# Kernel optimization log

Hardware: AMD Instinct MI355X
Metric: run time of the kernel (lower is better)

The kernel has to match this reference:

```python
import jax, jax.numpy as jnp
import numpy as np

B, LC, LQ, H = 64, 1024, 128, 512
NEG = -1e30


def setup_inputs() -> dict:
    key = jax.random.key(0)
    ks = jax.random.split(key, 12)
    s = 1.0 / np.sqrt(H)
    return {
        "c": jax.random.normal(ks[0], (B, LC, H), jnp.float32),
        "q": jax.random.normal(ks[1], (B, LQ, H), jnp.float32),
        "c_mask": jax.random.randint(ks[2], (B, LC), 0, 2, jnp.int32),
        "q_mask": jax.random.randint(ks[3], (B, LQ), 0, 2, jnp.int32),
        "c_weight": jax.random.normal(ks[4], (H, 1), jnp.float32) * s,
        "q_weight": jax.random.normal(ks[5], (H, 1), jnp.float32) * s,
        "cq_weight": jax.random.normal(ks[6], (1, 1, H), jnp.float32) * s,
        "bias": jnp.zeros((1,), jnp.float32),
        "W1": jax.random.normal(ks[7], (H, H), jnp.float32) * s,
        "b1": jnp.zeros((H,), jnp.float32),
        "W2": jax.random.normal(ks[8], (H, H), jnp.float32) * s,
        "b2": jnp.zeros((H,), jnp.float32),
    }


def reference(c, q, c_mask, q_mask, c_weight, q_weight, cq_weight, bias, W1, b1, W2, b2):
    # --- trilinear similarity (BiDAF eq. 1, memory-efficient form) ---
    s0 = c @ c_weight                                   # [B, LC, 1]
    s1 = jnp.swapaxes(q @ q_weight, 1, 2)               # [B, 1, LQ]
    s2 = jnp.einsum('bch,bqh->bcq', c * cq_weight, q)   # [B, LC, LQ]
    sim = s0 + s1 + s2 + bias

    qm = (q_mask != 0)[:, None, :]   # [B, 1, LQ]
    cm = (c_mask != 0)[:, :, None]   # [B, LC, 1]

    # dual masked softmax (dropout is identity in eval mode)
    s1s = jax.nn.softmax(jnp.where(qm, sim, NEG), axis=2)  # c2q weights
    s2s = jax.nn.softmax(jnp.where(cm, sim, NEG), axis=1)  # q2c weights

    a = s1s @ q                                            # [B, LC, H]
    b = jnp.einsum('bcq,bkq->bck', s1s, s2s) @ c           # [B, LC, H]

    # co-attention branch: qprime = relu(lin2(relu(lin1(q))))
    qp = jax.nn.relu(jax.nn.relu(q @ W1 + b1) @ W2 + b2)   # [B, LQ, H]
    scoat = jnp.einsum('bch,bqh->bcq', c, qp)              # [B, LC, LQ]
    sc1 = jax.nn.softmax(jnp.where(qm, scoat, NEG), axis=2)
    sc2 = jax.nn.softmax(jnp.where(cm, scoat, NEG), axis=1)
    acoat = sc1 @ qp                                       # [B, LC, H]
    bcoat = jnp.einsum('bcq,bch->bqh', sc2, c)             # [B, LQ, H]
    scoat3 = sc1 @ bcoat                                   # [B, LC, H]

    return jnp.concatenate([c, a, c * a, c * b, scoat3, acoat], axis=2)  # [B, LC, 6H]
```

## Files before the change

kernel.cpp:

```cpp
#include <hip/hip_runtime.h>
#include <cstdint>
#include <cstddef>

typedef short    bf16x8 __attribute__((ext_vector_type(8)));
typedef _Float16 f16x8  __attribute__((ext_vector_type(8)));
typedef float    f32x4  __attribute__((ext_vector_type(4)));

#define NEGV (-1e30f)
#define LDT 40

__device__ __forceinline__ short f2bf(float x){
    union { float f; unsigned u; } v; v.f = x;
    return (short)((v.u + 0x7fffu + ((v.u >> 16) & 1u)) >> 16);
}
__device__ __forceinline__ float bf2f(short h){
    union { float f; unsigned u; } v; v.u = ((unsigned)(unsigned short)h) << 16; return v.f;
}
__device__ __forceinline__ short f2h(float x){
    _Float16 h = (_Float16)x;
    union { _Float16 h; unsigned short u; } v; v.h = h;
    return (short)v.u;
}
__device__ __forceinline__ unsigned packh(float a, float b){
    return (unsigned)(unsigned short)f2h(a) | ((unsigned)(unsigned short)f2h(b) << 16);
}
__device__ __forceinline__ int p64(int x){ return ((x & 3) << 4) | (x >> 2); }

__global__ __launch_bounds__(256)
void k_prep_w(const float* __restrict__ W1, const float* __restrict__ W2,
              short* __restrict__ W1Th, short* __restrict__ W1Tl,
              short* __restrict__ W2Th, short* __restrict__ W2Tl)
{
    int idx = blockIdx.x * 256 + threadIdx.x;
    int w = idx >> 18;
    int e = idx & ((1 << 18) - 1);
    int n = e & 511, k = e >> 9;
    const float* W = w ? W2 : W1;
    float x = W[k * 512 + n];
    short hi = f2bf(x);
    short lo = f2bf(x - bf2f(hi));
    size_t o = (size_t)n * 512 + k;
    if (w) { W2Th[o] = hi; W2Tl[o] = lo; } else { W1Th[o] = hi; W1Tl[o] = lo; }
}

__global__ __launch_bounds__(256)
void k_prep_q(const float* __restrict__ q, const float* __restrict__ qwv,
              const float* __restrict__ cqw, short* __restrict__ q_cq,
              short* __restrict__ qT, float* __restrict__ s1p)
{
    __shared__ short TT[128 * 136];
    __shared__ float qws[128], cqs[128];
    const int t = threadIdx.x;
    const int b = (int)(blockIdx.x >> 2), hb = (int)(blockIdx.x & 3), h0 = hb * 128;
    if (t < 128) { qws[t] = qwv[h0 + t]; cqs[t] = cqw[h0 + t]; }
    __syncthreads();
    #pragma unroll
    for (int it = 0; it < 16; it++) {
        int idx = it * 256 + t;
        int m = idx >> 5, c4 = (idx & 31) * 4;
        float4 v = *(const float4*)(q + ((size_t)b * 128 + m) * 512 + h0 + c4);
        TT[(c4 + 0) * 136 + m] = f2h(v.x);
        TT[(c4 + 1) * 136 + m] = f2h(v.y);
        TT[(c4 + 2) * 136 + m] = f2h(v.z);
        TT[(c4 + 3) * 136 + m] = f2h(v.w);
        uint2 d;
        d.x = packh(v.x * cqs[c4],     v.y * cqs[c4 + 1]);
        d.y = packh(v.z * cqs[c4 + 2], v.w * cqs[c4 + 3]);
        *(uint2*)(q_cq + ((size_t)b * 128 + m) * 512 + h0 + c4) = d;
        float dot = v.x * qws[c4] + v.y * qws[c4 + 1] + v.z * qws[c4 + 2] + v.w * qws[c4 + 3];
        #pragma unroll
        for (int off = 1; off < 32; off <<= 1) dot += __shfl_xor(dot, off);
        if ((t & 31) == 0) s1p[((size_t)b * 4 + hb) * 128 + m] = dot;
    }
    __syncthreads();
    const int h = t >> 1, half = t & 1;
    const int hm = (h & 64) + p64(h & 63);
    short* dst = qT + ((size_t)b * 512 + h0 + hm) * 128 + half * 64;
    #pragma unroll
    for (int j = 0; j < 8; j++)
        *(bf16x8*)(dst + j * 8) = *(const bf16x8*)&TT[h * 136 + half * 64 + j * 8];
}

template<bool WT>
__global__ __launch_bounds__(256)
void k_linear(const float* __restrict__ X, const short* __restrict__ WTh,
              const short* __restrict__ WTl, const float* __restrict__ bias,
              float* __restrict__ Y, short* __restrict__ Yf,
              short* __restrict__ YT)
{
    __shared__ __align__(16) short SMEM[4 * 128 * LDT];
    short* Ah = SMEM;
    short* Al = SMEM + 128 * LDT;
    short* Bh = SMEM + 2 * 128 * LDT;
    short* Bl = SMEM + 3 * 128 * LDT;
    const int t = threadIdx.x;
    const int m0 = (int)(blockIdx.x >> 2) * 128;
    const int n0 = (int)(blockIdx.x & 3) * 128;
    const int lane = t & 63;
    const int wr = (t >> 7) & 1, wc = (t >> 6) & 1;
    const int fr = lane & 15, fg = lane >> 4;
    const int srow = t >> 1, sk = (t & 1) * 16;

    f32x4 acc[4][4] = {};

    for (int k0 = 0; k0 < 512; k0 += 32) {
        __syncthreads();
        {
            const float* src = X + (size_t)(m0 + srow) * 512 + k0 + sk;
            float4 f[4];
            #pragma unroll
            for (int i = 0; i < 4; i++) f[i] = ((const float4*)src)[i];
            const float* fv = (const float*)f;
            short hi[16], lo[16];
            #pragma unroll
            for (int j = 0; j < 16; j++) {
                float x = fv[j];
                short h = f2bf(x);
                hi[j] = h; lo[j] = f2bf(x - bf2f(h));
            }
            #pragma unroll
            for (int j = 0; j < 2; j++) {
                *(bf16x8*)&Ah[srow * LDT + sk + j * 8] = *(bf16x8*)&hi[j * 8];
                *(bf16x8*)&Al[srow * LDT + sk + j * 8] = *(bf16x8*)&lo[j * 8];
            }
        }
        {
            const short* sh = WTh + (size_t)(n0 + srow) * 512 + k0 + sk;
            const short* sl = WTl + (size_t)(n0 + srow) * 512 + k0 + sk;
            #pragma unroll
            for (int j = 0; j < 2; j++) {
                *(bf16x8*)&Bh[srow * LDT + sk + j * 8] = ((const bf16x8*)sh)[j];
                *(bf16x8*)&Bl[srow * LDT + sk + j * 8] = ((const bf16x8*)sl)[j];
            }
        }
        __syncthreads();
        bf16x8 a_h[4], a_l[4], b_h[4], b_l[4];
        #pragma unroll
        for (int i = 0; i < 4; i++) {
            int ar = (wr * 64 + i * 16 + fr) * LDT + fg * 8;
            int br = (wc * 64 + i * 16 + fr) * LDT + fg * 8;
            a_h[i] = *(const bf16x8*)&Ah[ar];
            a_l[i] = *(const bf16x8*)&Al[ar];
            b_h[i] = *(const bf16x8*)&Bh[br];
            b_l[i] = *(const bf16x8*)&Bl[br];
        }
        #pragma unroll
        for (int mi = 0; mi < 4; mi++)
        #pragma unroll
        for (int ni = 0; ni < 4; ni++) {
            acc[mi][ni] = __builtin_amdgcn_mfma_f32_16x16x32_bf16(a_h[mi], b_h[ni], acc[mi][ni], 0, 0, 0);
            acc[mi][ni] = __builtin_amdgcn_mfma_f32_16x16x32_bf16(a_h[mi], b_l[ni], acc[mi][ni], 0, 0, 0);
            acc[mi][ni] = __builtin_amdgcn_mfma_f32_16x16x32_bf16(a_l[mi], b_h[ni], acc[mi][ni], 0, 0, 0);
        }
    }
    float bv[4];
    #pragma unroll
    for (int ni = 0; ni < 4; ni++) bv[ni] = bias[n0 + wc * 64 + ni * 16 + fr];

    if (!WT) {
        #pragma unroll
        for (int mi = 0; mi < 4; mi++)
        #pragma unroll
        for (int r = 0; r < 4; r++) {
            int row = m0 + wr * 64 + mi * 16 + fg * 4 + r;
            #pragma unroll
            for (int ni = 0; ni < 4; ni++)
                Y[(size_t)row * 512 + n0 + wc * 64 + ni * 16 + fr] =
                    fmaxf(acc[mi][ni][r] + bv[ni], 0.f);
        }
    } else {
        #pragma unroll
        for (int mi = 0; mi < 4; mi++)
        #pragma unroll
        for (int r = 0; r < 4; r++) {
            int row = m0 + wr * 64 + mi * 16 + fg * 4 + r;
            #pragma unroll
            for (int ni = 0; ni < 4; ni++) {
                float v = fmaxf(acc[mi][ni][r] + bv[ni], 0.f);
                size_t o = (size_t)row * 512 + n0 + wc * 64 + ni * 16 + fr;
                Yf[o] = f2h(v);
            }
        }
        __syncthreads();
        short* TT = SMEM;
        #pragma unroll
        for (int mi = 0; mi < 4; mi++)
        #pragma unroll
        for (int r = 0; r < 4; r++) {
            int ml = wr * 64 + mi * 16 + fg * 4 + r;
            #pragma unroll
            for (int ni = 0; ni < 4; ni++)
                TT[(wc * 64 + ni * 16 + fr) * 136 + ml] =
                    f2h(fmaxf(acc[mi][ni][r] + bv[ni], 0.f));
        }
        __syncthreads();
        const int n = t >> 1, half = t & 1;
        const int nm = (n & 64) + p64(n & 63);
        short* dst = YT + ((size_t)(m0 >> 7) * 512 + n0 + nm) * 128 + half * 64;
        #pragma unroll
        for (int j = 0; j < 8; j++)
            *(bf16x8*)(dst + j * 8) = *(const bf16x8*)&TT[n * 136 + half * 64 + j * 8];
    }
}

template<bool ADDS>
__global__ __launch_bounds__(256)
void k_att(const float* __restrict__ Cc, const short* __restrict__ Bhg,
           const float* __restrict__ cwv, const float* __restrict__ s1pg,
           const float* __restrict__ biasp, const int* __restrict__ qmask,
           const int* __restrict__ cmask, short* __restrict__ Pr,
           short* __restrict__ Pe, float2* __restrict__ colpart)
{
    __shared__ __align__(16) short SM[128 * 136];
    short* Ah = SM;
    short* Bh = SM + 128 * LDT;
    short* TT = SM;
    __shared__ float red[2][128];
    __shared__ float mrowL[128], rinvL[128], cmaxL[128];
    __shared__ float cws[ADDS ? 512 : 1];
    __shared__ float s0red[ADDS ? 128 : 1][2];
    __shared__ float s0L[ADDS ? 128 : 1], s1L[ADDS ? 128 : 1];
    __shared__ int qmsL[128], cmsL[128];

    const int t = threadIdx.x;
    const int b  = (int)(blockIdx.x & 63);
    const int ch = (int)(blockIdx.x >> 6);
    const int m0 = ch * 128;
    const int lane = t & 63;
    const int wr = (t >> 7) & 1, wc = (t >> 6) & 1;
    const int fr = lane & 15, fg = lane >> 4;
    const int srow = t >> 1, sk = (t & 1) * 16;

    if (ADDS) { cws[t] = cwv[t]; cws[t + 256] = cwv[t + 256]; }
    if (t < 128) {
        qmsL[t] = qmask[b * 128 + t];
        cmsL[t] = cmask[b * 1024 + m0 + t];
        if (ADDS)
            s1L[t] = s1pg[((size_t)b * 4 + 0) * 128 + t] + s1pg[((size_t)b * 4 + 1) * 128 + t]
                   + s1pg[((size_t)b * 4 + 2) * 128 + t] + s1pg[((size_t)b * 4 + 3) * 128 + t];
    }

    const size_t aoff = ((size_t)b * 1024 + m0 + srow) * 512;
    const size_t boff = ((size_t)b * 128 + srow) * 512;
    float s0part = 0.f;
    f32x4 acc[4][4] = {};

    for (int k0 = 0; k0 < 512; k0 += 32) {
        __syncthreads();
        {
            const float* src = Cc + aoff + k0 + sk;
            float4 f[4];
            #pragma unroll
            for (int i = 0; i < 4; i++) f[i] = ((const float4*)src)[i];
            const float* fv = (const float*)f;
            short hv[16];
            #pragma unroll
            for (int j = 0; j < 16; j++) {
                float x = fv[j];
                if (ADDS) s0part += x * cws[k0 + sk + j];
                hv[j] = f2h(x);
            }
            #pragma unroll
            for (int j = 0; j < 2; j++)
                *(bf16x8*)&Ah[srow * LDT + sk + j * 8] = *(bf16x8*)&hv[j * 8];
        }
        {
            *(uint4*)&Bh[srow * LDT + sk]     = *(const uint4*)(Bhg + boff + k0 + sk);
            *(uint4*)&Bh[srow * LDT + sk + 8] = *(const uint4*)(Bhg + boff + k0 + sk + 8);
        }
        __syncthreads();
        #pragma unroll
        for (int i = 0; i < 4; i++) {
            f16x8 a_ = *(const f16x8*)&Ah[(wr * 64 + i * 16 + fr) * LDT + fg * 8];
            #pragma unroll
            for (int ni = 0; ni < 4; ni++) {
                f16x8 b_ = *(const f16x8*)&Bh[(wc * 64 + ni * 16 + fr) * LDT + fg * 8];
                acc[i][ni] = __builtin_amdgcn_mfma_f32_16x16x32_f16(a_, b_, acc[i][ni], 0, 0, 0);
            }
        }
    }

    if (ADDS) {
        s0red[srow][t & 1] = s0part;
        __syncthreads();
        if (t < 128) s0L[t] = s0red[t][0] + s0red[t][1];
        __syncthreads();
        float b0 = biasp[0];
        #pragma unroll
        for (int mi = 0; mi < 4; mi++)
        #pragma unroll
        for (int r = 0; r < 4; r++) {
            float s0r = s0L[wr * 64 + mi * 16 + fg * 4 + r] + b0;
            #pragma unroll
            for (int ni = 0; ni < 4; ni++)
                acc[mi][ni][r] += s0r + s1L[wc * 64 + ni * 16 + fr];
        }
    }

    bool qmv[4];
    #pragma unroll
    for (int ni = 0; ni < 4; ni++) qmv[ni] = qmsL[wc * 64 + ni * 16 + fr] != 0;
    bool cmb[4][4];
    #pragma unroll
    for (int mi = 0; mi < 4; mi++)
    #pragma unroll
    for (int r = 0; r < 4; r++) cmb[mi][r] = cmsL[wr * 64 + mi * 16 + fg * 4 + r] != 0;

    #pragma unroll
    for (int mi = 0; mi < 4; mi++)
    #pragma unroll
    for (int r = 0; r < 4; r++) {
        float m = NEGV;
        #pragma unroll
        for (int ni = 0; ni < 4; ni++) if (qmv[ni]) m = fmaxf(m, acc[mi][ni][r]);
        #pragma unroll
        for (int off = 1; off < 16; off <<= 1) m = fmaxf(m, __shfl_xor(m, off));
        if (fr == 0) red[wc][wr * 64 + mi * 16 + fg * 4 + r] = m;
    }
    __syncthreads();
    if (t < 128) mrowL[t] = fmaxf(red[0][t], red[1][t]);
    __syncthreads();
    #pragma unroll
    for (int mi = 0; mi < 4; mi++)
    #pragma unroll
    for (int r = 0; r < 4; r++) {
        float mr = mrowL[wr * 64 + mi * 16 + fg * 4 + r];
        float s = 0.f;
        #pragma unroll
        for (int ni = 0; ni < 4; ni++) if (qmv[ni]) s += __expf(acc[mi][ni][r] - mr);
        #pragma unroll
        for (int off = 1; off < 16; off <<= 1) s += __shfl_xor(s, off);
        if (fr == 0) red[wc][wr * 64 + mi * 16 + fg * 4 + r] = s;
    }
    __syncthreads();
    if (t < 128) rinvL[t] = 1.f / (red[0][t] + red[1][t]);
    __syncthreads();
    #pragma unroll
    for (int mi = 0; mi < 4; mi++)
    #pragma unroll
    for (int r = 0; r < 4; r++) {
        int rowl = wr * 64 + mi * 16 + fg * 4 + r;
        float mr = mrowL[rowl], iv = rinvL[rowl];
        size_t obase = ((size_t)b * 1024 + m0 + rowl) * 128;
        #pragma unroll
        for (int ni = 0; ni < 4; ni++) {
            float o = qmv[ni] ? __expf(acc[mi][ni][r] - mr) * iv : 0.f;
            Pr[obase + wc * 64 + ni * 16 + fr] = f2h(o);
        }
    }

    float cpart[4];
    #pragma unroll
    for (int ni = 0; ni < 4; ni++) {
        float m = NEGV;
        #pragma unroll
        for (int mi = 0; mi < 4; mi++)
        #pragma unroll
        for (int r = 0; r < 4; r++) if (cmb[mi][r]) m = fmaxf(m, acc[mi][ni][r]);
        m = fmaxf(m, __shfl_xor(m, 16));
        m = fmaxf(m, __shfl_xor(m, 32));
        cpart[ni] = m;
    }
    if (fg == 0) {
        #pragma unroll
        for (int ni = 0; ni < 4; ni++) red[wr][wc * 64 + ni * 16 + fr] = cpart[ni];
    }
    __syncthreads();
    if (t < 128) cmaxL[t] = fmaxf(red[0][t], red[1][t]);
    __syncthreads();
    #pragma unroll
    for (int ni = 0; ni < 4; ni++) {
        const int q = wc * 64 + ni * 16 + fr;
        float cm = cmaxL[q];
        float s = 0.f;
        #pragma unroll
        for (int mi = 0; mi < 4; mi++)
        #pragma unroll
        for (int r = 0; r < 4; r++) {
            int rloc = wr * 64 + mi * 16 + fg * 4 + r;
            float e = cmb[mi][r] ? __expf(acc[mi][ni][r] - cm) : 0.f;
            s += e;
            TT[q * 136 + rloc] = f2h(e);
        }
        s += __shfl_xor(s, 16);
        s += __shfl_xor(s, 32);
        cpart[ni] = s;
    }
    __syncthreads();
    if (fg == 0) {
        #pragma unroll
        for (int ni = 0; ni < 4; ni++) red[wr][wc * 64 + ni * 16 + fr] = cpart[ni];
    }
    __syncthreads();
    {
        const int q2 = t >> 1, half = t & 1;
        short* dst = Pe + ((size_t)b * 128 + q2) * 1024 + m0 + half * 64;
        #pragma unroll
        for (int j = 0; j < 8; j++)
            *(bf16x8*)(dst + j * 8) = *(const bf16x8*)&TT[q2 * 136 + half * 64 + j * 8];
    }
    if (t < 128) colpart[((size_t)b * 8 + ch) * 128 + t] = make_float2(cmaxL[t], red[0][t] + red[1][t]);
}

__global__ __launch_bounds__(256)
void k_kgemm2(const short* __restrict__ A1, const short* __restrict__ A2,
              const float* __restrict__ Cc, const float2* __restrict__ cpS,
              const float2* __restrict__ cpC, short* __restrict__ Y1T,
              short* __restrict__ Y2T)
{
    __shared__ __align__(16) short Bs[2][64 * LDT];
    __shared__ __align__(16) short TT[64 * 136];
    __shared__ float wtr[2][8][128];
    __shared__ float fin[2][128];
    const int t = threadIdx.x;
    const int b  = (int)(blockIdx.x & 63);
    const int n0 = (int)(blockIdx.x >> 6) * 64;
    const int lane = t & 63;
    const int w  = t >> 6;
    const int wr = w >> 1, wc = w & 1;
    const int fr = lane & 15, fg = lane >> 4;
    const int n4 = (t & 15) * 4, kk2 = (t >> 4) * 2;

    {
        const int tb = t >> 7, qq = t & 127;
        const float2* cp = tb ? cpC : cpS;
        float2 pc[8];
        #pragma unroll
        for (int c2 = 0; c2 < 8; c2++) pc[c2] = cp[((size_t)b * 8 + c2) * 128 + qq];
        float Mg = NEGV;
        #pragma unroll
        for (int c2 = 0; c2 < 8; c2++) Mg = fmaxf(Mg, pc[c2].x);
        float Sg = 0.f;
        #pragma unroll
        for (int c2 = 0; c2 < 8; c2++) Sg += pc[c2].y * __expf(pc[c2].x - Mg);
        const float clampv = Mg - 60.f;
        float mh[8];
        #pragma unroll
        for (int c2 = 0; c2 < 8; c2++) mh[c2] = fmaxf(pc[c2].x, clampv);
        wtr[tb][0][qq] = 1.f;
        #pragma unroll
        for (int c2 = 1; c2 < 8; c2++) wtr[tb][c2][qq] = __expf(mh[c2 - 1] - mh[c2]);
        fin[tb][qq] = (Sg > 0.f) ? __expf(mh[7] - Mg) / Sg : 0.f;
    }

    f32x4 acc1[4][2] = {}, acc2[4][2] = {};

    auto load_e = [&](int k0, float4* e) {
        const float* p = Cc + ((size_t)b * 1024 + k0 + kk2) * 512 + n0 + n4;
        e[0] = *(const float4*)(p);
        e[1] = *(const float4*)(p + 512);
    };
    auto store_b = [&](const float4* e, int buf) {
        const float* p0 = (const float*)&e[0];
        const float* p1 = (const float*)&e[1];
        #pragma unroll
        for (int l = 0; l < 4; l++)
            *(unsigned*)&Bs[buf][(n4 + l) * LDT + kk2] = packh(p0[l], p1[l]);
    };

    {
        float4 e[2];
        load_e(0, e);
        store_b(e, 0);
    }
    __syncthreads();

    for (int k0 = 0; k0 < 1024; k0 += 32) {
        const int cur = (k0 >> 5) & 1;
        const bool more = (k0 + 32) < 1024;
        float4 e[2];
        if (more) load_e(k0 + 32, e);
        if (k0 && (k0 & 127) == 0) {
            const int c2 = k0 >> 7;
            #pragma unroll
            for (int mi = 0; mi < 4; mi++)
            #pragma unroll
            for (int r = 0; r < 4; r++) {
                int qq = wr * 64 + mi * 16 + fg * 4 + r;
                float f1 = wtr[0][c2][qq], f2 = wtr[1][c2][qq];
                #pragma unroll
                for (int ni = 0; ni < 2; ni++) {
                    acc1[mi][ni][r] *= f1;
                    acc2[mi][ni][r] *= f2;
                }
            }
        }
        f16x8 a1[4], a2[4], bg[2];
        #pragma unroll
        for (int i = 0; i < 4; i++) {
            size_t arow = (size_t)(b * 128 + wr * 64 + i * 16 + fr) * 1024 + k0 + fg * 8;
            a1[i] = *(const f16x8*)(A1 + arow);
            a2[i] = *(const f16x8*)(A2 + arow);
        }
        #pragma unroll
        for (int i = 0; i < 2; i++)
            bg[i] = *(const f16x8*)&Bs[cur][(wc * 32 + i * 16 + fr) * LDT + fg * 8];
        #pragma unroll
        for (int mi = 0; mi < 4; mi++)
        #pragma unroll
        for (int ni = 0; ni < 2; ni++) {
            acc1[mi][ni] = __builtin_amdgcn_mfma_f32_16x16x32_f16(a1[mi], bg[ni], acc1[mi][ni], 0, 0, 0);
            acc2[mi][ni] = __builtin_amdgcn_mfma_f32_16x16x32_f16(a2[mi], bg[ni], acc2[mi][ni], 0, 0, 0);
        }
        if (more) store_b(e, cur ^ 1);
        __syncthreads();
    }

    const int n_l = t >> 2, qu = t & 3;
    const int nm = p64(n_l);
    #pragma unroll
    for (int mi = 0; mi < 4; mi++)
    #pragma unroll
    for (int r = 0; r < 4; r++) {
        int ml = wr * 64 + mi * 16 + fg * 4 + r;
        float fs = fin[0][ml];
        #pragma unroll
        for (int ni = 0; ni < 2; ni++)
            TT[(wc * 32 + ni * 16 + fr) * 136 + ml] = f2h(acc1[mi][ni][r] * fs);
    }
    __syncthreads();
    {
        short* dst = Y1T + ((size_t)b * 512 + n0 + nm) * 128 + qu * 32;
        #pragma unroll
        for (int j = 0; j < 4; j++)
            *(bf16x8*)(dst + j * 8) = *(const bf16x8*)&TT[n_l * 136 + qu * 32 + j * 8];
    }
    __syncthreads();
    #pragma unroll
    for (int mi = 0; mi < 4; mi++)
    #pragma unroll
    for (int r = 0; r < 4; r++) {
        int ml = wr * 64 + mi * 16 + fg * 4 + r;
        float fs = fin[1][ml];
        #pragma unroll
        for (int ni = 0; ni < 2; ni++)
            TT[(wc * 32 + ni * 16 + fr) * 136 + ml] = f2h(acc2[mi][ni][r] * fs);
    }
    __syncthreads();
    {
        short* dst = Y2T + ((size_t)b * 512 + n0 + nm) * 128 + qu * 32;
        #pragma unroll
        for (int j = 0; j < 4; j++)
            *(bf16x8*)(dst + j * 8) = *(const bf16x8*)&TT[n_l * 136 + qu * 32 + j * 8];
    }
}

template<bool WITHC>
__global__ __launch_bounds__(256)
void k_epi(const short* __restrict__ Pm, const short* __restrict__ BT1,
           const short* __restrict__ BT2, const float* __restrict__ Cc,
           float* __restrict__ out)
{
    const int t = threadIdx.x;
    const int hb = (int)(blockIdx.x & 3);
    const int mb = (int)((blockIdx.x >> 2) & 7);
    const int b  = (int)(blockIdx.x >> 5);
    const int m0 = mb * 128, h0 = hb * 128;
    const int lane = t & 63;
    const int wr = (t >> 7) & 1, wc = (t >> 6) & 1;
    const int fr = lane & 15, fg = lane >> 4;
    f32x4 acc1[4][4] = {}, acc2[4][4] = {};
    const short* Abase  = Pm  + ((size_t)b * 1024 + m0) * 128;
    const short* B1base = BT1 + ((size_t)b * 512 + h0) * 128;
    const short* B2base = BT2 + ((size_t)b * 512 + h0) * 128;
    #pragma unroll
    for (int kk = 0; kk < 4; kk++) {
        const int k0 = kk * 32;
        f16x8 af[4], b1[4], b2[4];
        #pragma unroll
        for (int i = 0; i < 4; i++) {
            af[i] = *(const f16x8*)(Abase  + (size_t)(wr * 64 + i * 16 + fr) * 128 + k0 + fg * 8);
            b1[i] = *(const f16x8*)(B1base + (size_t)(wc * 64 + i * 16 + fr) * 128 + k0 + fg * 8);
            b2[i] = *(const f16x8*)(B2base + (size_t)(wc * 64 + i * 16 + fr) * 128 + k0 + fg * 8);
        }
        #pragma unroll
        for (int mi = 0; mi < 4; mi++)
        #pragma unroll
        for (int ni = 0; ni < 4; ni++) {
            acc1[mi][ni] = __builtin_amdgcn_mfma_f32_16x16x32_f16(af[mi], b1[ni], acc1[mi][ni], 0, 0, 0);
            acc2[mi][ni] = __builtin_amdgcn_mfma_f32_16x16x32_f16(af[mi], b2[ni], acc2[mi][ni], 0, 0, 0);
        }
    }
    const size_t crow_base = (size_t)b * 1024 + m0;
    const int colb = wc * 64 + fr * 4;
    #pragma unroll
    for (int mi = 0; mi < 4; mi++)
    #pragma unroll
    for (int r = 0; r < 4; r++) {
        int rowl = wr * 64 + mi * 16 + fg * 4 + r;
        size_t obase = (crow_base + rowl) * 3072 + h0 + colb;
        float4 av, bv;
        av.x = acc1[mi][0][r]; av.y = acc1[mi][1][r]; av.z = acc1[mi][2][r]; av.w = acc1[mi][3][r];
        bv.x = acc2[mi][0][r]; bv.y = acc2[mi][1][r]; bv.z = acc2[mi][2][r]; bv.w = acc2[mi][3][r];
        if (WITHC) {
            float4 cv = *(const float4*)(Cc + (crow_base + rowl) * 512 + h0 + colb);
            *(float4*)(out + obase) = cv;
            *(float4*)(out + obase + 512) = av;
            float4 ca; ca.x = cv.x * av.x; ca.y = cv.y * av.y; ca.z = cv.z * av.z; ca.w = cv.w * av.w;
            *(float4*)(out + obase + 1024) = ca;
            float4 cb; cb.x = cv.x * bv.x; cb.y = cv.y * bv.y; cb.z = cv.z * bv.z; cb.w = cv.w * bv.w;
            *(float4*)(out + obase + 1536) = cb;
        } else {
            *(float4*)(out + obase + 2048) = bv;
            *(float4*)(out + obase + 2560) = av;
        }
    }
}

extern "C" void kernel_launch(void* const* d_in, const int* in_sizes, int n_in,
                              void* d_out, int out_size, void* d_ws, size_t ws_size,
                              hipStream_t stream)
{
    const float* c     = (const float*)d_in[0];
    const float* q     = (const float*)d_in[1];
    const int*   cmask = (const int*)d_in[2];
    const int*   qmask = (const int*)d_in[3];
    const float* cwv   = (const float*)d_in[4];
    const float* qwv   = (const float*)d_in[5];
    const float* cqw   = (const float*)d_in[6];
    const float* bias  = (const float*)d_in[7];
    const float* W1    = (const float*)d_in[8];
    const float* b1    = (const float*)d_in[9];
    const float* W2    = (const float*)d_in[10];
    const float* b2    = (const float*)d_in[11];
    float* out = (float*)d_out;

    char* ws = (char*)d_ws;
    size_t off = 0;
    auto alloc = [&](size_t bytes) -> char* {
        char* p = ws + off;
        off = (off + bytes + 255) & ~(size_t)255;
        return p;
    };
    short* w1th = (short*)alloc(512 * 512 * 2);
    short* w1tl = (short*)alloc(512 * 512 * 2);
    short* w2th = (short*)alloc(512 * 512 * 2);
    short* w2tl = (short*)alloc(512 * 512 * 2);
    float* s1p  = (float*)alloc(64 * 4 * 128 * 4);
    short* q_cq = (short*)alloc((size_t)64 * 128 * 512 * 2);
    short* qT   = (short*)alloc((size_t)64 * 512 * 128 * 2);
    float* z1   = (float*)alloc((size_t)8192 * 512 * 4);
    short* qp_f = (short*)alloc((size_t)8192 * 512 * 2);
    short* qpT  = (short*)alloc((size_t)64 * 512 * 128 * 2);
    float2* colpartS = (float2*)alloc((size_t)64 * 8 * 128 * 8);
    float2* colpartC = (float2*)alloc((size_t)64 * 8 * 128 * 8);
    short* s1s  = (short*)alloc((size_t)64 * 1024 * 128 * 2);
    short* s2sT = (short*)alloc((size_t)64 * 128 * 1024 * 2);
    short* sc1  = (short*)alloc((size_t)64 * 1024 * 128 * 2);
    short* sc2T = (short*)alloc((size_t)64 * 128 * 1024 * 2);
    short* binT = (short*)z1;
    short* bcoT = ((short*)z1) + (size_t)64 * 512 * 128;

    k_prep_w<<<2048, 256, 0, stream>>>(W1, W2, w1th, w1tl, w2th, w2tl);
    k_prep_q<<<256, 256, 0, stream>>>(q, qwv, cqw, q_cq, qT, s1p);
    k_linear<false><<<256, 256, 0, stream>>>(q, w1th, w1tl, b1, z1, nullptr, nullptr);
    k_linear<true><<<256, 256, 0, stream>>>(z1, w2th, w2tl, b2, nullptr, qp_f, qpT);

    k_att<true><<<512, 256, 0, stream>>>(
        c, q_cq, cwv, s1p, bias, qmask, cmask, s1s, s2sT, colpartS);

    k_att<false><<<512, 256, 0, stream>>>(
        c, qp_f, nullptr, nullptr, nullptr, qmask, cmask, sc1, sc2T, colpartC);

    k_kgemm2<<<512, 256, 0, stream>>>(s2sT, sc2T, c, colpartS, colpartC, binT, bcoT);

    k_epi<true><<<2048, 256, 0, stream>>>(s1s, qT, binT, c, out);
    k_epi<false><<<2048, 256, 0, stream>>>(sc1, qpT, bcoT, nullptr, out);
}
```

Before: 571.4 us.

## Fuse both attention GEMMs into one kernel and cache c as fp16

The two k_att launches are merged into one k_att_dual kernel. It loads each tile of c once, runs MFMAs against both the q_cq and qp operands, and then runs the dual-softmax emit for each result. While staging, it also writes an fp16 copy of c to workspace, and k_kgemm2 and k_epi read that copy instead of the fp32 c. This is meant to cut repeated fp32 reads of c and conversion work. In exchange it doubles accumulator registers per thread, adds a 64 MB workspace write, and makes the copied c slice of the output lose precision through fp16 rounding.

```diff
diff --git a/kernel.cpp b/kernel.cpp
--- a/kernel.cpp
+++ b/kernel.cpp
@@ -4,6 +4,7 @@
 
 typedef short    bf16x8 __attribute__((ext_vector_type(8)));
 typedef _Float16 f16x8  __attribute__((ext_vector_type(8)));
+typedef _Float16 f16x4  __attribute__((ext_vector_type(4)));
 typedef float    f32x4  __attribute__((ext_vector_type(4)));
 
 #define NEGV (-1e30f)
@@ -203,23 +204,25 @@
     }
 }
 
-template<bool ADDS>
-__global__ __launch_bounds__(256)
-void k_att(const float* __restrict__ Cc, const short* __restrict__ Bhg,
-           const float* __restrict__ cwv, const float* __restrict__ s1pg,
-           const float* __restrict__ biasp, const int* __restrict__ qmask,
-           const int* __restrict__ cmask, short* __restrict__ Pr,
-           short* __restrict__ Pe, float2* __restrict__ colpart)
+__global__ __launch_bounds__(256, 2)
+void k_att_dual(const float* __restrict__ Cc, const short* __restrict__ B1g,
+                const short* __restrict__ B2g, const float* __restrict__ cwv,
+                const float* __restrict__ s1pg, const float* __restrict__ biasp,
+                const int* __restrict__ qmask, const int* __restrict__ cmask,
+                short* __restrict__ c16,
+                short* __restrict__ Pr1, short* __restrict__ Pe1, float2* __restrict__ cp1,
+                short* __restrict__ Pr2, short* __restrict__ Pe2, float2* __restrict__ cp2)
 {
     __shared__ __align__(16) short SM[128 * 136];
-    short* Ah = SM;
-    short* Bh = SM + 128 * LDT;
-    short* TT = SM;
+    short* Ah  = SM;
+    short* B1h = SM + 128 * LDT;
+    short* B2h = SM + 2 * 128 * LDT;
+    short* TT  = SM;
     __shared__ float red[2][128];
     __shared__ float mrowL[128], rinvL[128], cmaxL[128];
-    __shared__ float cws[ADDS ? 512 : 1];
-    __shared__ float s0red[ADDS ? 128 : 1][2];
-    __shared__ float s0L[ADDS ? 128 : 1], s1L[ADDS ? 128 : 1];
+    __shared__ float cws[512];
+    __shared__ float s0red[128][2];
+    __shared__ float s0L[128], s1L[128];
     __shared__ int qmsL[128], cmsL[128];
 
     const int t = threadIdx.x;
@@ -231,19 +234,18 @@
     const int fr = lane & 15, fg = lane >> 4;
     const int srow = t >> 1, sk = (t & 1) * 16;
 
-    if (ADDS) { cws[t] = cwv[t]; cws[t + 256] = cwv[t + 256]; }
+    cws[t] = cwv[t]; cws[t + 256] = cwv[t + 256];
     if (t < 128) {
         qmsL[t] = qmask[b * 128 + t];
         cmsL[t] = cmask[b * 1024 + m0 + t];
-        if (ADDS)
-            s1L[t] = s1pg[((size_t)b * 4 + 0) * 128 + t] + s1pg[((size_t)b * 4 + 1) * 128 + t]
-                   + s1pg[((size_t)b * 4 + 2) * 128 + t] + s1pg[((size_t)b * 4 + 3) * 128 + t];
+        s1L[t] = s1pg[((size_t)b * 4 + 0) * 128 + t] + s1pg[((size_t)b * 4 + 1) * 128 + t]
+               + s1pg[((size_t)b * 4 + 2) * 128 + t] + s1pg[((size_t)b * 4 + 3) * 128 + t];
     }
 
     const size_t aoff = ((size_t)b * 1024 + m0 + srow) * 512;
     const size_t boff = ((size_t)b * 128 + srow) * 512;
     float s0part = 0.f;
-    f32x4 acc[4][4] = {};
+    f32x4 acc1[4][4] = {}, acc2[4][4] = {};
 
     for (int k0 = 0; k0 < 512; k0 += 32) {
         __syncthreads();
@@ -257,16 +259,20 @@
             #pragma unroll
             for (int j = 0; j < 16; j++) {
                 float x = fv[j];
-                if (ADDS) s0part += x * cws[k0 + sk + j];
+                s0part += x * cws[k0 + sk + j];
                 hv[j] = f2h(x);
             }
             #pragma unroll
-            for (int j = 0; j < 2; j++)
+            for (int j = 0; j < 2; j++) {
                 *(bf16x8*)&Ah[srow * LDT + sk + j * 8] = *(bf16x8*)&hv[j * 8];
+                *(bf16x8*)(c16 + aoff + k0 + sk + j * 8) = *(bf16x8*)&hv[j * 8];
+            }
         }
         {
-            *(uint4*)&Bh[srow * LDT + sk]     = *(const uint4*)(Bhg + boff + k0 + sk);
-            *(uint4*)&Bh[srow * LDT + sk + 8] = *(const uint4*)(Bhg + boff + k0 + sk + 8);
+            *(uint4*)&B1h[srow * LDT + sk]     = *(const uint4*)(B1g + boff + k0 + sk);
+            *(uint4*)&B1h[srow * LDT + sk + 8] = *(const uint4*)(B1g + boff + k0 + sk + 8);
+            *(uint4*)&B2h[srow * LDT + sk]     = *(const uint4*)(B2g + boff + k0 + sk);
+            *(uint4*)&B2h[srow * LDT + sk + 8] = *(const uint4*)(B2g + boff + k0 + sk + 8);
         }
         __syncthreads();
         #pragma unroll
@@ -274,17 +280,20 @@
             f16x8 a_ = *(const f16x8*)&Ah[(wr * 64 + i * 16 + fr) * LDT + fg * 8];
             #pragma unroll
             for (int ni = 0; ni < 4; ni++) {
-                f16x8 b_ = *(const f16x8*)&Bh[(wc * 64 + ni * 16 + fr) * LDT + fg * 8];
-                acc[i][ni] = __builtin_amdgcn_mfma_f32_16x16x32_f16(a_, b_, acc[i][ni], 0, 0, 0);
-            }
-        }
-    }
-
-    if (ADDS) {
-        s0red[srow][t & 1] = s0part;
-        __syncthreads();
-        if (t < 128) s0L[t] = s0red[t][0] + s0red[t][1];
-        __syncthreads();
+                int br = (wc * 64 + ni * 16 + fr) * LDT + fg * 8;
+                f16x8 b1_ = *(const f16x8*)&B1h[br];
+                acc1[i][ni] = __builtin_amdgcn_mfma_f32_16x16x32_f16(a_, b1_, acc1[i][ni], 0, 0, 0);
+                f16x8 b2_ = *(const f16x8*)&B2h[br];
+                acc2[i][ni] = __builtin_amdgcn_mfma_f32_16x16x32_f16(a_, b2_, acc2[i][ni], 0, 0, 0);
+            }
+        }
+    }
+
+    s0red[srow][t & 1] = s0part;
+    __syncthreads();
+    if (t < 128) s0L[t] = s0red[t][0] + s0red[t][1];
+    __syncthreads();
+    {
         float b0 = biasp[0];
         #pragma unroll
         for (int mi = 0; mi < 4; mi++)
@@ -293,7 +302,7 @@
             float s0r = s0L[wr * 64 + mi * 16 + fg * 4 + r] + b0;
             #pragma unroll
             for (int ni = 0; ni < 4; ni++)
-                acc[mi][ni][r] += s0r + s1L[wc * 64 + ni * 16 + fr];
+                acc1[mi][ni][r] += s0r + s1L[wc * 64 + ni * 16 + fr];
         }
     }
 
@@ -306,105 +315,111 @@
     #pragma unroll
     for (int r = 0; r < 4; r++) cmb[mi][r] = cmsL[wr * 64 + mi * 16 + fg * 4 + r] != 0;
 
-    #pragma unroll
-    for (int mi = 0; mi < 4; mi++)
-    #pragma unroll
-    for (int r = 0; r < 4; r++) {
-        float m = NEGV;
-        #pragma unroll
-        for (int ni = 0; ni < 4; ni++) if (qmv[ni]) m = fmaxf(m, acc[mi][ni][r]);
-        #pragma unroll
-        for (int off = 1; off < 16; off <<= 1) m = fmaxf(m, __shfl_xor(m, off));
-        if (fr == 0) red[wc][wr * 64 + mi * 16 + fg * 4 + r] = m;
-    }
-    __syncthreads();
-    if (t < 128) mrowL[t] = fmaxf(red[0][t], red[1][t]);
-    __syncthreads();
-    #pragma unroll
-    for (int mi = 0; mi < 4; mi++)
-    #pragma unroll
-    for (int r = 0; r < 4; r++) {
-        float mr = mrowL[wr * 64 + mi * 16 + fg * 4 + r];
-        float s = 0.f;
-        #pragma unroll
-        for (int ni = 0; ni < 4; ni++) if (qmv[ni]) s += __expf(acc[mi][ni][r] - mr);
-        #pragma unroll
-        for (int off = 1; off < 16; off <<= 1) s += __shfl_xor(s, off);
-        if (fr == 0) red[wc][wr * 64 + mi * 16 + fg * 4 + r] = s;
-    }
-    __syncthreads();
-    if (t < 128) rinvL[t] = 1.f / (red[0][t] + red[1][t]);
-    __syncthreads();
-    #pragma unroll
-    for (int mi = 0; mi < 4; mi++)
-    #pragma unroll
-    for (int r = 0; r < 4; r++) {
-        int rowl = wr * 64 + mi * 16 + fg * 4 + r;
-        float mr = mrowL[rowl], iv = rinvL[rowl];
-        size_t obase = ((size_t)b * 1024 + m0 + rowl) * 128;
+    auto emit = [&](f32x4 (&acc)[4][4], short* __restrict__ Pr,
+                    short* __restrict__ Pe, float2* __restrict__ cpart_g) {
+        __syncthreads();
+        #pragma unroll
+        for (int mi = 0; mi < 4; mi++)
+        #pragma unroll
+        for (int r = 0; r < 4; r++) {
+            float m = NEGV;
+            #pragma unroll
+            for (int ni = 0; ni < 4; ni++) if (qmv[ni]) m = fmaxf(m, acc[mi][ni][r]);
+            #pragma unroll
+            for (int off = 1; off < 16; off <<= 1) m = fmaxf(m, __shfl_xor(m, off));
+            if (fr == 0) red[wc][wr * 64 + mi * 16 + fg * 4 + r] = m;
+        }
+        __syncthreads();
+        if (t < 128) mrowL[t] = fmaxf(red[0][t], red[1][t]);
+        __syncthreads();
+        #pragma unroll
+        for (int mi = 0; mi < 4; mi++)
+        #pragma unroll
+        for (int r = 0; r < 4; r++) {
+            float mr = mrowL[wr * 64 + mi * 16 + fg * 4 + r];
+            float s = 0.f;
+            #pragma unroll
+            for (int ni = 0; ni < 4; ni++) if (qmv[ni]) s += __expf(acc[mi][ni][r] - mr);
+            #pragma unroll
+            for (int off = 1; off < 16; off <<= 1) s += __shfl_xor(s, off);
+            if (fr == 0) red[wc][wr * 64 + mi * 16 + fg * 4 + r] = s;
+        }
+        __syncthreads();
+        if (t < 128) rinvL[t] = 1.f / (red[0][t] + red[1][t]);
+        __syncthreads();
+        #pragma unroll
+        for (int mi = 0; mi < 4; mi++)
+        #pragma unroll
+        for (int r = 0; r < 4; r++) {
+            int rowl = wr * 64 + mi * 16 + fg * 4 + r;
+            float mr = mrowL[rowl], iv = rinvL[rowl];
+            size_t obase = ((size_t)b * 1024 + m0 + rowl) * 128;
+            #pragma unroll
+            for (int ni = 0; ni < 4; ni++) {
+                float o = qmv[ni] ? __expf(acc[mi][ni][r] - mr) * iv : 0.f;
+                Pr[obase + wc * 64 + ni * 16 + fr] = f2h(o);
+            }
+        }
+        float cpart[4];
         #pragma unroll
         for (int ni = 0; ni < 4; ni++) {
-            float o = qmv[ni] ? __expf(acc[mi][ni][r] - mr) * iv : 0.f;
-            Pr[obase + wc * 64 + ni * 16 + fr] = f2h(o);
-        }
-    }
-
-    float cpart[4];
-    #pragma unroll
-    for (int ni = 0; ni < 4; ni++) {
-        float m = NEGV;
-        #pragma unroll
-        for (int mi = 0; mi < 4; mi++)
-        #pragma unroll
-        for (int r = 0; r < 4; r++) if (cmb[mi][r]) m = fmaxf(m, acc[mi][ni][r]);
-        m = fmaxf(m, __shfl_xor(m, 16));
-        m = fmaxf(m, __shfl_xor(m, 32));
-        cpart[ni] = m;
-    }
-    if (fg == 0) {
-        #pragma unroll
-        for (int ni = 0; ni < 4; ni++) red[wr][wc * 64 + ni * 16 + fr] = cpart[ni];
-    }
-    __syncthreads();
-    if (t < 128) cmaxL[t] = fmaxf(red[0][t], red[1][t]);
-    __syncthreads();
-    #pragma unroll
-    for (int ni = 0; ni < 4; ni++) {
-        const int q = wc * 64 + ni * 16 + fr;
-        float cm = cmaxL[q];
-        float s = 0.f;
-        #pragma unroll
-        for (int mi = 0; mi < 4; mi++)
-        #pragma unroll
-        for (int r = 0; r < 4; r++) {
-            int rloc = wr * 64 + mi * 16 + fg * 4 + r;
-            float e = cmb[mi][r] ? __expf(acc[mi][ni][r] - cm) : 0.f;
-            s += e;
-            TT[q * 136 + rloc] = f2h(e);
-        }
-        s += __shfl_xor(s, 16);
-        s += __shfl_xor(s, 32);
-        cpart[ni] = s;
-    }
-    __syncthreads();
-    if (fg == 0) {
-        #pragma unroll
-        for (int ni = 0; ni < 4; ni++) red[wr][wc * 64 + ni * 16 + fr] = cpart[ni];
-    }
-    __syncthreads();
-    {
-        const int q2 = t >> 1, half = t & 1;
-        short* dst = Pe + ((size_t)b * 128 + q2) * 1024 + m0 + half * 64;
-        #pragma unroll
-        for (int j = 0; j < 8; j++)
-            *(bf16x8*)(dst + j * 8) = *(const bf16x8*)&TT[q2 * 136 + half * 64 + j * 8];
-    }
-    if (t < 128) colpart[((size_t)b * 8 + ch) * 128 + t] = make_float2(cmaxL[t], red[0][t] + red[1][t]);
+            float m = NEGV;
+            #pragma unroll
+            for (int mi = 0; mi < 4; mi++)
+            #pragma unroll
+            for (int r = 0; r < 4; r++) if (cmb[mi][r]) m = fmaxf(m, acc[mi][ni][r]);
+            m = fmaxf(m, __shfl_xor(m, 16));
+            m = fmaxf(m, __shfl_xor(m, 32));
+            cpart[ni] = m;
+        }
+        if (fg == 0) {
+            #pragma unroll
+            for (int ni = 0; ni < 4; ni++) red[wr][wc * 64 + ni * 16 + fr] = cpart[ni];
+        }
+        __syncthreads();
+        if (t < 128) cmaxL[t] = fmaxf(red[0][t], red[1][t]);
+        __syncthreads();
+        #pragma unroll
+        for (int ni = 0; ni < 4; ni++) {
+            const int q = wc * 64 + ni * 16 + fr;
+            float cm = cmaxL[q];
+            float s = 0.f;
+            #pragma unroll
+            for (int mi = 0; mi < 4; mi++)
+            #pragma unroll
+            for (int r = 0; r < 4; r++) {
+                int rloc = wr * 64 + mi * 16 + fg * 4 + r;
+                float e = cmb[mi][r] ? __expf(acc[mi][ni][r] - cm) : 0.f;
+                s += e;
+                TT[q * 136 + rloc] = f2h(e);
+            }
+            s += __shfl_xor(s, 16);
+            s += __shfl_xor(s, 32);
+            cpart[ni] = s;
+        }
+        __syncthreads();
+        if (fg == 0) {
+            #pragma unroll
+            for (int ni = 0; ni < 4; ni++) red[wr][wc * 64 + ni * 16 + fr] = cpart[ni];
+        }
+        __syncthreads();
+        {
+            const int q2 = t >> 1, half = t & 1;
+            short* dst = Pe + ((size_t)b * 128 + q2) * 1024 + m0 + half * 64;
+            #pragma unroll
+            for (int j = 0; j < 8; j++)
+                *(bf16x8*)(dst + j * 8) = *(const bf16x8*)&TT[q2 * 136 + half * 64 + j * 8];
+        }
+        if (t < 128) cpart_g[((size_t)b * 8 + ch) * 128 + t] = make_float2(cmaxL[t], red[0][t] + red[1][t]);
+    };
+
+    emit(acc1, Pr1, Pe1, cp1);
+    emit(acc2, Pr2, Pe2, cp2);
 }
 
 __global__ __launch_bounds__(256)
 void k_kgemm2(const short* __restrict__ A1, const short* __restrict__ A2,
-              const float* __restrict__ Cc, const float2* __restrict__ cpS,
+              const short* __restrict__ C16, const float2* __restrict__ cpS,
               const float2* __restrict__ cpC, short* __restrict__ Y1T,
               short* __restrict__ Y2T)
 {
@@ -445,21 +460,21 @@
 
     f32x4 acc1[4][2] = {}, acc2[4][2] = {};
 
-    auto load_e = [&](int k0, float4* e) {
-        const float* p = Cc + ((size_t)b * 1024 + k0 + kk2) * 512 + n0 + n4;
-        e[0] = *(const float4*)(p);
-        e[1] = *(const float4*)(p + 512);
+    auto load_e = [&](int k0, uint2* e) {
+        const short* p = C16 + ((size_t)b * 1024 + k0 + kk2) * 512 + n0 + n4;
+        e[0] = *(const uint2*)(p);
+        e[1] = *(const uint2*)(p + 512);
     };
-    auto store_b = [&](const float4* e, int buf) {
-        const float* p0 = (const float*)&e[0];
-        const float* p1 = (const float*)&e[1];
+    auto store_b = [&](const uint2* e, int buf) {
+        const unsigned short* r0 = (const unsigned short*)&e[0];
+        const unsigned short* r1 = (const unsigned short*)&e[1];
         #pragma unroll
         for (int l = 0; l < 4; l++)
-            *(unsigned*)&Bs[buf][(n4 + l) * LDT + kk2] = packh(p0[l], p1[l]);
+            *(unsigned*)&Bs[buf][(n4 + l) * LDT + kk2] = (unsigned)r0[l] | ((unsigned)r1[l] << 16);
     };
 
     {
-        float4 e[2];
+        uint2 e[2];
         load_e(0, e);
         store_b(e, 0);
     }
@@ -468,7 +483,7 @@
     for (int k0 = 0; k0 < 1024; k0 += 32) {
         const int cur = (k0 >> 5) & 1;
         const bool more = (k0 + 32) < 1024;
-        float4 e[2];
+        uint2 e[2];
         if (more) load_e(k0 + 32, e);
         if (k0 && (k0 & 127) == 0) {
             const int c2 = k0 >> 7;
@@ -548,7 +563,7 @@
 template<bool WITHC>
 __global__ __launch_bounds__(256)
 void k_epi(const short* __restrict__ Pm, const short* __restrict__ BT1,
-           const short* __restrict__ BT2, const float* __restrict__ Cc,
+           const short* __restrict__ BT2, const short* __restrict__ C16,
            float* __restrict__ out)
 {
     const int t = threadIdx.x;
@@ -593,7 +608,9 @@
         av.x = acc1[mi][0][r]; av.y = acc1[mi][1][r]; av.z = acc1[mi][2][r]; av.w = acc1[mi][3][r];
         bv.x = acc2[mi][0][r]; bv.y = acc2[mi][1][r]; bv.z = acc2[mi][2][r]; bv.w = acc2[mi][3][r];
         if (WITHC) {
-            float4 cv = *(const float4*)(Cc + (crow_base + rowl) * 512 + h0 + colb);
+            f16x4 cv4 = *(const f16x4*)(C16 + (crow_base + rowl) * 512 + h0 + colb);
+            float4 cv;
+            cv.x = (float)cv4[0]; cv.y = (float)cv4[1]; cv.z = (float)cv4[2]; cv.w = (float)cv4[3];
             *(float4*)(out + obase) = cv;
             *(float4*)(out + obase + 512) = av;
             float4 ca; ca.x = cv.x * av.x; ca.y = cv.y * av.y; ca.z = cv.z * av.z; ca.w = cv.w * av.w;
@@ -642,6 +659,7 @@
     float* z1   = (float*)alloc((size_t)8192 * 512 * 4);
     short* qp_f = (short*)alloc((size_t)8192 * 512 * 2);
     short* qpT  = (short*)alloc((size_t)64 * 512 * 128 * 2);
+    short* c16  = (short*)alloc((size_t)64 * 1024 * 512 * 2);
     float2* colpartS = (float2*)alloc((size_t)64 * 8 * 128 * 8);
     float2* colpartC = (float2*)alloc((size_t)64 * 8 * 128 * 8);
     short* s1s  = (short*)alloc((size_t)64 * 1024 * 128 * 2);
@@ -656,14 +674,12 @@
     k_linear<false><<<256, 256, 0, stream>>>(q, w1th, w1tl, b1, z1, nullptr, nullptr);
     k_linear<true><<<256, 256, 0, stream>>>(z1, w2th, w2tl, b2, nullptr, qp_f, qpT);
 
-    k_att<true><<<512, 256, 0, stream>>>(
-        c, q_cq, cwv, s1p, bias, qmask, cmask, s1s, s2sT, colpartS);
-
-    k_att<false><<<512, 256, 0, stream>>>(
-        c, qp_f, nullptr, nullptr, nullptr, qmask, cmask, sc1, sc2T, colpartC);
-
-    k_kgemm2<<<512, 256, 0, stream>>>(s2sT, sc2T, c, colpartS, colpartC, binT, bcoT);
-
-    k_epi<true><<<2048, 256, 0, stream>>>(s1s, qT, binT, c, out);
+    k_att_dual<<<512, 256, 0, stream>>>(
+        c, q_cq, qp_f, cwv, s1p, bias, qmask, cmask, c16,
+        s1s, s2sT, colpartS, sc1, sc2T, colpartC);
+
+    k_kgemm2<<<512, 256, 0, stream>>>(s2sT, sc2T, c16, colpartS, colpartC, binT, bcoT);
+
+    k_epi<true><<<2048, 256, 0, stream>>>(s1s, qT, binT, c16, out);
     k_epi<false><<<2048, 256, 0, stream>>>(sc1, qpT, bcoT, nullptr, out);
 }
```

Result: no change. 569.1 us, median of 2 (-0.4%).
